# Optimization experiments

Hardware: AMD Instinct MI355X
Metric: run time of the kernel (lower is better)

The kernel has to match this reference:

```python
import jax, jax.numpy as jnp
import numpy as np

N_NODES = 100_000
E_OFF = 1_500_000
LATENT = 64
MP_STEPS = 3


def setup_inputs() -> dict:
    key = jax.random.key(0)
    ks = jax.random.split(key, 12)
    # lower-triangular graph: all self-loops + random off-diagonal edges with row >= col
    r = jax.random.randint(ks[0], (E_OFF,), 0, N_NODES)
    c = jax.random.randint(ks[1], (E_OFF,), 0, N_NODES)
    diag = jnp.arange(N_NODES)
    edge_row = jnp.concatenate([jnp.maximum(r, c), diag]).astype(jnp.int64)
    edge_col = jnp.concatenate([jnp.minimum(r, c), diag]).astype(jnp.int64)
    E = E_OFF + N_NODES
    # positive weights (gcn_norm takes deg^{-1/2} of weighted degree)
    edge_attr = jax.random.uniform(ks[2], (E,), jnp.float32) + 0.05
    x = jax.random.normal(ks[3], (N_NODES, 1), jnp.float32)
    L = LATENT
    def lin(k, fi, fo):
        return jax.random.normal(k, (fi, fo), jnp.float32) / np.sqrt(fi)
    return {
        "x": x,
        "edge_attr": edge_attr,
        "w_enc": lin(ks[4], 1, L), "b_enc": jnp.zeros((L,), jnp.float32),
        "conv1_w": jax.random.normal(ks[5], (MP_STEPS, L, L), jnp.float32) / np.sqrt(L),
        "conv1_b": jnp.zeros((MP_STEPS, L), jnp.float32),
        "conv2_w": jax.random.normal(ks[6], (MP_STEPS, L, L), jnp.float32) / np.sqrt(L),
        "conv2_b": jnp.zeros((MP_STEPS, L), jnp.float32),
        "dec_w1": lin(ks[7], 2 * L, L), "dec_b1": jnp.zeros((L,), jnp.float32),
        "dec_w2": lin(ks[8], L, 1), "dec_b2": jnp.zeros((1,), jnp.float32),
        "edge_row": edge_row,
        "edge_col": edge_col,
    }


def reference(x, edge_attr, w_enc, b_enc, conv1_w, conv1_b, conv2_w, conv2_b,
              dec_w1, dec_b1, dec_w2, dec_b2, edge_row, edge_col):
    N = x.shape[0]
    # GCN normalization (graph already contains all self-loops, so PyG's
    # add_remaining_self_loops is a no-op and keeps existing loop weights)
    deg = jax.ops.segment_sum(edge_attr, edge_col, num_segments=N)
    dinv = jnp.where(deg > 0, jax.lax.rsqrt(jnp.maximum(deg, 1e-30)), 0.0)
    norm = dinv[edge_row] * edge_attr * dinv[edge_col]  # [E]
    cnt = jnp.maximum(
        jax.ops.segment_sum(jnp.ones_like(edge_attr), edge_col, num_segments=N), 1.0
    )[:, None]  # mean aggregation denominator

    def gcn(h, W, b):
        m = (h @ W)[edge_row] * norm[:, None]           # [E, F] messages
        agg = jax.ops.segment_sum(m, edge_col, num_segments=N) / cnt
        return agg + b

    # node encoder: single Linear (no activation)
    h = x @ w_enc + b_enc
    for i in range(MP_STEPS):
        h = jax.nn.relu(gcn(h, conv1_w[i], conv1_b[i]))
        h = jax.nn.relu(gcn(h, conv2_w[i], conv2_b[i]))

    # edge decoder: gather endpoints, MLP [2L -> L -> 1]
    e = jnp.concatenate([h[edge_row], h[edge_col]], axis=1)
    e = jax.nn.relu(e @ dec_w1 + dec_b1)
    e = (e @ dec_w2 + dec_b2)[:, 0]                      # [E]
    vals = jnp.where(edge_row == edge_col, jax.nn.softplus(e), e)
    return vals
```

## Files before the change

### kernel.cpp

```cpp
#include <hip/hip_runtime.h>
#include <hip/hip_fp16.h>
#include <math.h>

#define L 64
#define FIXS 65536.0f
#define WAITCNT_LGKM0 0xC07F

#define FMAMIX_LO(acc, pkh, ws) \
    asm("v_fma_mix_f32 %0, %1, %2, %0 op_sel:[0,0,0] op_sel_hi:[1,0,0]" \
        : "+v"(acc) : "v"(pkh), "v"(ws))
#define FMAMIX_HI(acc, pkh, ws) \
    asm("v_fma_mix_f32 %0, %1, %2, %0 op_sel:[1,0,0] op_sel_hi:[1,0,0]" \
        : "+v"(acc) : "v"(pkh), "v"(ws))
#define PKADDRELU(d, a, b) \
    asm("v_pk_add_f16 %0, %1, %2\n\tv_pk_max_f16 %0, %0, 0" \
        : "=v"(d) : "v"(a), "v"(b))

#define GLOAD(xw_, qv_, J) \
    xw_ = (unsigned)__shfl((int)mwv, (J) * 8 + grp); \
    qv_ = h4[(size_t)(xw_ & 0x1FFFFu) * 8 + sub];
#define FMA8(A, qv_, xw_) { \
    float wv_ = __half2float(__ushort_as_half((unsigned short)((xw_) >> 17))); \
    FMAMIX_LO(A[0], (qv_).x, wv_); FMAMIX_HI(A[1], (qv_).x, wv_); \
    FMAMIX_LO(A[2], (qv_).y, wv_); FMAMIX_HI(A[3], (qv_).y, wv_); \
    FMAMIX_LO(A[4], (qv_).z, wv_); FMAMIX_HI(A[5], (qv_).z, wv_); \
    FMAMIX_LO(A[6], (qv_).w, wv_); FMAMIX_HI(A[7], (qv_).w, wv_); }


__global__ void k_hist(const int* __restrict__ col, const float* __restrict__ attr,
                       unsigned* __restrict__ degcnt,
                       int* __restrict__ rank, int E) {
    int e = blockIdx.x * blockDim.x + threadIdx.x;
    if (e < E) {
        int c = col[e];
        unsigned fx = (unsigned)(int)rintf(attr[e] * FIXS);
        unsigned old = atomicAdd(&degcnt[c], (1u << 24) | fx);
        rank[e] = (int)(old >> 24);
    }
}

__global__ void k_dinv(const unsigned* __restrict__ degcnt,
                       float* __restrict__ dinv, int* __restrict__ cntI,
                       float* __restrict__ rcnt, int N) {
    int n = blockIdx.x * blockDim.x + threadIdx.x;
    if (n < N) {
        unsigned p = degcnt[n];
        unsigned cnt = p >> 24;
        float d = (float)(p & 0xFFFFFFu) * (1.0f / FIXS);
        dinv[n] = (d > 0.f) ? (1.0f / sqrtf(fmaxf(d, 1e-30f))) : 0.f;
        cntI[n] = (int)cnt;
        unsigned c = cnt ? cnt : 1u;
        rcnt[n] = 1.0f / (float)c;
    }
}


__global__ __launch_bounds__(256) void k_scan_a(const int* __restrict__ cntI,
                                                int* __restrict__ blockSums, int N) {
    __shared__ int red[4];
    int b = blockIdx.x, t = threadIdx.x;
    int base = b * 1024 + t * 4;
    int s = 0;
    #pragma unroll
    for (int i = 0; i < 4; ++i) { int idx = base + i; if (idx < N) s += cntI[idx]; }
    #pragma unroll
    for (int off = 32; off > 0; off >>= 1) s += __shfl_down(s, off);
    if ((t & 63) == 0) red[t >> 6] = s;
    __syncthreads();
    if (t == 0) blockSums[b] = red[0] + red[1] + red[2] + red[3];
}

__global__ __launch_bounds__(1024) void k_scan_b(int* __restrict__ blockSums, int B,
                                                 int* __restrict__ ptr, int N) {
    __shared__ int sh[1024];
    int t = threadIdx.x;
    sh[t] = (t < B) ? blockSums[t] : 0;
    __syncthreads();
    for (int off = 1; off < 1024; off <<= 1) {
        int v = (t >= off) ? sh[t - off] : 0;
        __syncthreads();
        sh[t] += v;
        __syncthreads();
    }
    if (t < B) blockSums[t] = (t == 0) ? 0 : sh[t - 1];
    if (t == B - 1) ptr[N] = sh[t];
}

__global__ __launch_bounds__(256) void k_scan_c(const int* __restrict__ cntI,
                                                const int* __restrict__ blockSums,
                                                int* __restrict__ ptr, int N) {
    __shared__ int th[256];
    int b = blockIdx.x, t = threadIdx.x;
    int base = b * 1024 + t * 4;
    int v[4]; int s = 0;
    #pragma unroll
    for (int i = 0; i < 4; ++i) {
        int idx = base + i;
        v[i] = (idx < N) ? cntI[idx] : 0;
        s += v[i];
    }
    th[t] = s;
    __syncthreads();
    for (int off = 1; off < 256; off <<= 1) {
        int xv = (t >= off) ? th[t - off] : 0;
        __syncthreads();
        th[t] += xv;
        __syncthreads();
    }
    int pre = ((t == 0) ? 0 : th[t - 1]) + blockSums[b];
    #pragma unroll
    for (int i = 0; i < 4; ++i) {
        int idx = base + i;
        if (idx < N) ptr[idx] = pre;
        pre += v[i];
    }
}

__global__ void k_scatter(const int* __restrict__ row, const int* __restrict__ col,
                          const float* __restrict__ attr, const float* __restrict__ dinv,
                          const int* __restrict__ colptr,
                          int* __restrict__ rank,
                          unsigned* __restrict__ csrX, int E) {
    int e = blockIdx.x * blockDim.x + threadIdx.x;
    if (e < E) {
        int r = row[e], c = col[e];
        int pos = colptr[c] + rank[e];
        float nrm = dinv[r] * attr[e] * dinv[c];
        unsigned short nb = __half_as_ushort(__float2half(nrm));
        csrX[pos] = (unsigned)r | ((unsigned)nb << 17);
        rank[e] = pos;
    }
}


__global__ __launch_bounds__(256) void k_fill(const int* __restrict__ colptr,
                                              int* __restrict__ colof, int N) {
    int lane = threadIdx.x & 63;
    int wid  = (blockIdx.x * blockDim.x + threadIdx.x) >> 6;
    int nw   = (gridDim.x * blockDim.x) >> 6;
    for (int n = wid; n < N; n += nw) {
        int beg = colptr[n], end = colptr[n + 1];
        for (int p = beg + lane; p < end; p += 64) colof[p] = n;
    }
}


__global__ void k_encode(const float* __restrict__ x, const float* __restrict__ w_enc,
                         const float* __restrict__ b_enc, __half* __restrict__ h, int N) {
    int idx = blockIdx.x * blockDim.x + threadIdx.x;
    if (idx < N * L) {
        int n = idx >> 6, f = idx & 63;
        h[idx] = __float2half(x[n] * w_enc[f] + b_enc[f]);
    }
}


__global__ __launch_bounds__(256, 2) void k_gcn(const uint4* __restrict__ h4,
        __half* __restrict__ h_out,
        const float* __restrict__ W, const float* __restrict__ bias,
        const int* __restrict__ colptr, const unsigned* __restrict__ csrX,
        const float* __restrict__ rcnt, int N) {
    __shared__ float sm[4][72];
    int lane = threadIdx.x & 63;
    int warp = threadIdx.x >> 6;
    int grp  = lane >> 3;
    int sub  = lane & 7;
    int wid  = (blockIdx.x * blockDim.x + threadIdx.x) >> 6;
    int nw   = (gridDim.x * blockDim.x) >> 6;
    float* smw = &sm[warp][0];

    float Wc[L];
    #pragma unroll
    for (int f = 0; f < L; ++f) Wc[f] = W[f * L + lane];
    #pragma unroll
    for (int f = 0; f < L; ++f) asm volatile("" : "+v"(Wc[f]));
    float bl = bias[lane];

    int beg = 0, end = 0; unsigned mw = 0;
    if (wid < N) {
        beg = colptr[wid];
        end = colptr[wid + 1];
        if (beg + lane < end) mw = csrX[beg + lane];
    }

    for (int n = wid; n < N; n += nw) {
        int n2 = n + nw;
        int beg2 = 0, end2 = 0;
        if (n2 < N) { beg2 = colptr[n2]; end2 = colptr[n2 + 1]; }
        float rcv = rcnt[n];

        float va[8];
        #pragma unroll
        for (int i = 0; i < 8; ++i) va[i] = 0.f;

        auto PROC = [&](unsigned mwv, int mm) {
            int kmax = (mm + 7) >> 3;
            int k = 0;
            while (k < kmax) {
                int rem = kmax - k;
                if (rem >= 4) {
                    unsigned x0, x1, x2, x3; uint4 q0, q1, q2, q3;
                    GLOAD(x0, q0, k) GLOAD(x1, q1, k + 1)
                    GLOAD(x2, q2, k + 2) GLOAD(x3, q3, k + 3)
                    FMA8(va, q0, x0) FMA8(va, q1, x1)
                    FMA8(va, q2, x2) FMA8(va, q3, x3)
                    k += 4;
                } else if (rem == 3) {
                    unsigned x0, x1, x2; uint4 q0, q1, q2;
                    GLOAD(x0, q0, k) GLOAD(x1, q1, k + 1) GLOAD(x2, q2, k + 2)
                    FMA8(va, q0, x0) FMA8(va, q1, x1) FMA8(va, q2, x2)
                    k += 3;
                } else if (rem == 2) {
                    unsigned x0, x1; uint4 q0, q1;
                    GLOAD(x0, q0, k) GLOAD(x1, q1, k + 1)
                    FMA8(va, q0, x0) FMA8(va, q1, x1)
                    k += 2;
                } else {
                    unsigned x0; uint4 q0;
                    GLOAD(x0, q0, k)
                    FMA8(va, q0, x0)
                    k += 1;
                }
            }
        };

        int m = end - beg; if (m > 64) m = 64;
        PROC(mw, m);
        for (int base = beg + 64; base < end; base += 64) {
            int mm = end - base; if (mm > 64) mm = 64;
            unsigned mwc = 0;
            if (lane < mm) mwc = csrX[base + lane];
            PROC(mwc, mm);
        }

        unsigned mw2 = 0;
        if (n2 < N && beg2 + lane < end2) mw2 = csrX[beg2 + lane];

        float s[8];
        #pragma unroll
        for (int i = 0; i < 8; ++i) {
            float v = va[i];
            v += __shfl_xor(v, 8);
            v += __shfl_xor(v, 16);
            v += __shfl_xor(v, 32);
            s[i] = v;
        }
        if (lane < 8) {
            #pragma unroll
            for (int i = 0; i < 8; ++i) smw[8 * lane + i] = s[i];
        }
        __builtin_amdgcn_s_waitcnt(WAITCNT_LGKM0);
        float a0 = 0.f, a1 = 0.f, a2 = 0.f, a3 = 0.f;
        const float4* smv = (const float4*)smw;
        #pragma unroll
        for (int q = 0; q < 16; ++q) {
            float4 sv = smv[q];
            a0 += sv.x * Wc[4 * q + 0];
            a1 += sv.y * Wc[4 * q + 1];
            a2 += sv.z * Wc[4 * q + 2];
            a3 += sv.w * Wc[4 * q + 3];
        }
        float o = ((a0 + a1) + (a2 + a3)) * rcv + bl;
        h_out[(size_t)n * L + lane] = __float2half(fmaxf(o, 0.f));

        beg = beg2; end = end2; mw = mw2;
    }
}


__global__ __launch_bounds__(256, 2) void k_mv2(const __half* __restrict__ h,
        const float* __restrict__ W1, const float* __restrict__ b1,
        __half* __restrict__ U, __half* __restrict__ V, int N) {
    __shared__ float sm[4][72];
    int lane = threadIdx.x & 63;
    int warp = threadIdx.x >> 6;
    int wid  = (blockIdx.x * blockDim.x + threadIdx.x) >> 6;
    int nw   = (gridDim.x * blockDim.x) >> 6;
    float* smw = &sm[warp][0];
    float Wu[L], Wv[L];
    #pragma unroll
    for (int f = 0; f < L; ++f) Wu[f] = W1[f * L + lane];
    #pragma unroll
    for (int f = 0; f < L; ++f) Wv[f] = W1[(L + f) * L + lane];
    float bl = b1[lane];
    for (int n = wid; n < N; n += nw) {
        float hl = __half2float(h[(size_t)n * L + lane]);
        smw[lane] = hl;
        __builtin_amdgcn_s_waitcnt(WAITCNT_LGKM0);
        float a0 = 0.f, a1 = 0.f, c0 = 0.f, c1 = 0.f;
        const float4* smv = (const float4*)smw;
        #pragma unroll
        for (int q = 0; q < 16; ++q) {
            float4 sv = smv[q];
            a0 += sv.x * Wu[4 * q + 0] ; a1 += sv.y * Wu[4 * q + 1];
            a0 += sv.z * Wu[4 * q + 2] ; a1 += sv.w * Wu[4 * q + 3];
            c0 += sv.x * Wv[4 * q + 0] ; c1 += sv.y * Wv[4 * q + 1];
            c0 += sv.z * Wv[4 * q + 2] ; c1 += sv.w * Wv[4 * q + 3];
        }
        U[(size_t)n * L + lane] = __float2half((a0 + a1) + bl);
        V[(size_t)n * L + lane] = __float2half(c0 + c1);
        __builtin_amdgcn_s_waitcnt(WAITCNT_LGKM0);
    }
}


__global__ __launch_bounds__(256, 8) void k_edge(const __half* __restrict__ U,
        const __half* __restrict__ V, const float* __restrict__ w2,
        const float* __restrict__ b2, const unsigned* __restrict__ csrX,
        const int* __restrict__ colof, float* __restrict__ tmp, int E) {
    int sub = threadIdx.x & 7;
    float w2f[8];
    #pragma unroll
    for (int i = 0; i < 8; ++i) w2f[i] = w2[8 * sub + i];
    float b2v = b2[0];
    int tid = blockIdx.x * blockDim.x + threadIdx.x;
    int np  = (gridDim.x * blockDim.x) >> 3;
    for (int p = tid >> 3; p < E; p += np) {
        unsigned md = csrX[p];
        int r = (int)(md & 0x1FFFFu);
        int n = colof[p];
        uint4 uq = ((const uint4*)(U + (size_t)r * L))[sub];
        uint4 vq = ((const uint4*)(V + (size_t)n * L))[sub];
        float p0 = 0.f, p1 = 0.f;
        #define DOT2X(uw_, vw_, B) { unsigned t_; \
            PKADDRELU(t_, (uw_), (vw_)); \
            FMAMIX_LO(p0, t_, w2f[B]); FMAMIX_HI(p1, t_, w2f[(B) + 1]); }
        DOT2X(uq.x, vq.x, 0) DOT2X(uq.y, vq.y, 2)
        DOT2X(uq.z, vq.z, 4) DOT2X(uq.w, vq.w, 6)
        #undef DOT2X
        float pd = p0 + p1;
        pd += __shfl_xor(pd, 1);
        pd += __shfl_xor(pd, 2);
        pd += __shfl_xor(pd, 4);
        if (sub == 0) tmp[p] = pd + b2v;
    }
}


__global__ void k_perm(const int* __restrict__ epos, const float* __restrict__ tmp,
                       const int* __restrict__ erow, const int* __restrict__ ecol,
                       float* __restrict__ out, int E) {
    int e = blockIdx.x * blockDim.x + threadIdx.x;
    if (e < E) {
        float val = tmp[epos[e]];
        if (erow[e] == ecol[e])
            val = fmaxf(val, 0.f) + log1pf(expf(-fabsf(val)));
        out[e] = val;
    }
}


extern "C" void kernel_launch(void* const* d_in, const int* in_sizes, int n_in,
                              void* d_out, int out_size, void* d_ws, size_t ws_size,
                              hipStream_t stream) {
    const float* x     = (const float*)d_in[0];
    const float* attr  = (const float*)d_in[1];
    const float* w_enc = (const float*)d_in[2];
    const float* b_enc = (const float*)d_in[3];
    const float* c1w   = (const float*)d_in[4];
    const float* c1b   = (const float*)d_in[5];
    const float* c2w   = (const float*)d_in[6];
    const float* c2b   = (const float*)d_in[7];
    const float* dw1   = (const float*)d_in[8];
    const float* db1   = (const float*)d_in[9];
    const float* dw2   = (const float*)d_in[10];
    const float* db2   = (const float*)d_in[11];
    const int*   erow  = (const int*)d_in[12];
    const int*   ecol  = (const int*)d_in[13];
    int N = in_sizes[0];
    int E = in_sizes[1];
    float* out = (float*)d_out;

    char* w = (char*)d_ws;
    auto alloc = [&](size_t bytes) {
        char* p = w; w += (bytes + 255) & ~(size_t)255; return p;
    };
    unsigned* degcnt = (unsigned*)alloc((size_t)N * 4);
    size_t zbytes = (size_t)(w - (char*)d_ws);
    float* dinv   = (float*)alloc((size_t)N * 4);
    int*   cntI   = (int*)  alloc((size_t)N * 4);
    float* rcnt   = (float*)alloc((size_t)N * 4);
    int*   colptr = (int*)  alloc((size_t)(N + 1) * 4);
    int*   bsums  = (int*)  alloc(((size_t)(N + 1023) / 1024 + 1) * 4);
    int*   rank   = (int*)  alloc((size_t)E * 4);
    unsigned* csrX = (unsigned*)alloc((size_t)E * 4);
    int*   colof  = (int*)  alloc((size_t)E * 4);
    float* tmp    = (float*)alloc((size_t)E * 4);
    __half* hA    = (__half*)alloc((size_t)N * L * 2);
    __half* hB    = (__half*)alloc((size_t)N * L * 2);
    __half* hU    = (__half*)alloc((size_t)N * L * 2);
    __half* hV    = (__half*)alloc((size_t)N * L * 2);
    (void)ws_size; (void)n_in; (void)out_size;

    (void)hipMemsetAsync(d_ws, 0, zbytes, stream);

    int eb = (E + 255) / 256;
    int nb = (N + 255) / 256;
    int B  = (N + 1023) / 1024;
    k_hist<<<eb, 256, 0, stream>>>(ecol, attr, degcnt, rank, E);
    k_dinv<<<nb, 256, 0, stream>>>(degcnt, dinv, cntI, rcnt, N);
    k_scan_a<<<B, 256, 0, stream>>>(cntI, bsums, N);
    k_scan_b<<<1, 1024, 0, stream>>>(bsums, B, colptr, N);
    k_scan_c<<<B, 256, 0, stream>>>(cntI, bsums, colptr, N);
    k_scatter<<<eb, 256, 0, stream>>>(erow, ecol, attr, dinv, colptr, rank, csrX, E);
    k_fill<<<1024, 256, 0, stream>>>(colptr, colof, N);
    k_encode<<<(N * L + 255) / 256, 256, 0, stream>>>(x, w_enc, b_enc, hA, N);

    __half* hin = hA; __half* hout = hB;
    for (int i = 0; i < 3; ++i) {
        k_gcn<<<2048, 256, 0, stream>>>((const uint4*)hin, hout, c1w + i * L * L,
                                        c1b + i * L, colptr, csrX, rcnt, N);
        __half* t = hin; hin = hout; hout = t;
        k_gcn<<<2048, 256, 0, stream>>>((const uint4*)hin, hout, c2w + i * L * L,
                                        c2b + i * L, colptr, csrX, rcnt, N);
        t = hin; hin = hout; hout = t;
    }
    k_mv2<<<2048, 256, 0, stream>>>(hin, dw1, db1, hU, hV, N);
    k_edge<<<2048, 256, 0, stream>>>(hU, hV, dw2, db2, csrX, colof, tmp, E);
    k_perm<<<eb, 256, 0, stream>>>(rank, tmp, erow, ecol, out, E);
}
```

Baseline: 632.1 us.

## Reorder GCN to transform-then-aggregate with MFMA node matmul kernel

Each GCN layer is restructured from aggregate-then-multiply into a per-node dense transform (h@W) followed by a pure sparse aggregation, using the linearity of the weighted sum. The dense transform runs in a new MFMA kernel that splits W into hi/lo fp16 parts to keep accuracy, and the encoder is folded into the first layer's weights. The aggregation kernel drops its 64-float register weight cache and the shared-memory reduction, so it can run at higher occupancy. The cost is five extra kernel launches and an extra N×64 fp16 round trip through memory per layer, plus one more fp16 rounding of the transformed features before the gather.

```diff
diff --git a/kernel.cpp b/kernel.cpp
--- a/kernel.cpp
+++ b/kernel.cpp
@@ -5,6 +5,9 @@
 #define L 64
 #define FIXS 65536.0f
 #define WAITCNT_LGKM0 0xC07F
+
+typedef _Float16 f16x8 __attribute__((ext_vector_type(8)));
+typedef float f32x4 __attribute__((ext_vector_type(4)));
 
 #define FMAMIX_LO(acc, pkh, ws) \
     asm("v_fma_mix_f32 %0, %1, %2, %0 op_sel:[0,0,0] op_sel_hi:[1,0,0]" \
@@ -115,6 +118,7 @@
         pre += v[i];
     }
 }
+
 
 __global__ void k_scatter(const int* __restrict__ row, const int* __restrict__ col,
                           const float* __restrict__ attr, const float* __restrict__ dinv,
@@ -145,36 +149,44 @@
 }
 
 
-__global__ void k_encode(const float* __restrict__ x, const float* __restrict__ w_enc,
-                         const float* __restrict__ b_enc, __half* __restrict__ h, int N) {
+__global__ void k_fold(const float* __restrict__ w_enc, const float* __restrict__ b_enc,
+                       const float* __restrict__ W1,
+                       float* __restrict__ we1, float* __restrict__ be1) {
+    int j = threadIdx.x;
+    if (j < L) {
+        float a = 0.f, b = 0.f;
+        for (int f = 0; f < L; ++f) {
+            float wv = W1[f * L + j];
+            a += w_enc[f] * wv;
+            b += b_enc[f] * wv;
+        }
+        we1[j] = a; be1[j] = b;
+    }
+}
+
+__global__ void k_encode(const float* __restrict__ x, const float* __restrict__ we1,
+                         const float* __restrict__ be1, __half* __restrict__ g, int N) {
     int idx = blockIdx.x * blockDim.x + threadIdx.x;
     if (idx < N * L) {
         int n = idx >> 6, f = idx & 63;
-        h[idx] = __float2half(x[n] * w_enc[f] + b_enc[f]);
-    }
-}
-
-
-__global__ __launch_bounds__(256, 2) void k_gcn(const uint4* __restrict__ h4,
-        __half* __restrict__ h_out,
-        const float* __restrict__ W, const float* __restrict__ bias,
+        g[idx] = __float2half(x[n] * we1[f] + be1[f]);
+    }
+}
+
+
+__global__ __launch_bounds__(256, 6) void k_agg(const uint4* __restrict__ h4,
+        __half* __restrict__ h_out, const float* __restrict__ bias,
         const int* __restrict__ colptr, const unsigned* __restrict__ csrX,
         const float* __restrict__ rcnt, int N) {
-    __shared__ float sm[4][72];
     int lane = threadIdx.x & 63;
-    int warp = threadIdx.x >> 6;
     int grp  = lane >> 3;
     int sub  = lane & 7;
     int wid  = (blockIdx.x * blockDim.x + threadIdx.x) >> 6;
     int nw   = (gridDim.x * blockDim.x) >> 6;
-    float* smw = &sm[warp][0];
-
-    float Wc[L];
-    #pragma unroll
-    for (int f = 0; f < L; ++f) Wc[f] = W[f * L + lane];
-    #pragma unroll
-    for (int f = 0; f < L; ++f) asm volatile("" : "+v"(Wc[f]));
-    float bl = bias[lane];
+
+    float bl8[8];
+    #pragma unroll
+    for (int i = 0; i < 8; ++i) bl8[i] = bias[8 * sub + i];
 
     int beg = 0, end = 0; unsigned mw = 0;
     if (wid < N) {
@@ -246,24 +258,65 @@
             s[i] = v;
         }
         if (lane < 8) {
+            unsigned u[4];
             #pragma unroll
-            for (int i = 0; i < 8; ++i) smw[8 * lane + i] = s[i];
-        }
-        __builtin_amdgcn_s_waitcnt(WAITCNT_LGKM0);
-        float a0 = 0.f, a1 = 0.f, a2 = 0.f, a3 = 0.f;
-        const float4* smv = (const float4*)smw;
+            for (int i = 0; i < 4; ++i) {
+                float oa = fmaxf(s[2 * i]     * rcv + bl8[2 * i],     0.f);
+                float ob = fmaxf(s[2 * i + 1] * rcv + bl8[2 * i + 1], 0.f);
+                u[i] = (unsigned)__half_as_ushort(__float2half(oa))
+                     | ((unsigned)__half_as_ushort(__float2half(ob)) << 16);
+            }
+            uint4 st; st.x = u[0]; st.y = u[1]; st.z = u[2]; st.w = u[3];
+            ((uint4*)h_out)[(size_t)n * 8 + lane] = st;
+        }
+
+        beg = beg2; end = end2; mw = mw2;
+    }
+}
+
+
+__global__ __launch_bounds__(256) void k_gx(const __half* __restrict__ h,
+        const float* __restrict__ W, __half* __restrict__ g, int N) {
+    int lane = threadIdx.x & 63;
+    int wid  = (blockIdx.x * blockDim.x + threadIdx.x) >> 6;
+    int nw   = (gridDim.x * blockDim.x) >> 6;
+    int r16  = lane & 15;
+    int q4   = lane >> 4;
+
+    f16x8 bh[4][2], bl[4][2];
+    #pragma unroll
+    for (int t = 0; t < 4; ++t)
         #pragma unroll
-        for (int q = 0; q < 16; ++q) {
-            float4 sv = smv[q];
-            a0 += sv.x * Wc[4 * q + 0];
-            a1 += sv.y * Wc[4 * q + 1];
-            a2 += sv.z * Wc[4 * q + 2];
-            a3 += sv.w * Wc[4 * q + 3];
-        }
-        float o = ((a0 + a1) + (a2 + a3)) * rcv + bl;
-        h_out[(size_t)n * L + lane] = __float2half(fmaxf(o, 0.f));
-
-        beg = beg2; end = end2; mw = mw2;
+        for (int ks = 0; ks < 2; ++ks)
+            #pragma unroll
+            for (int i = 0; i < 8; ++i) {
+                int k = ks * 32 + q4 * 8 + i;
+                float wv = W[k * L + t * 16 + r16];
+                _Float16 hi = (_Float16)wv;
+                bh[t][ks][i] = hi;
+                bl[t][ks][i] = (_Float16)(wv - (float)hi);
+            }
+
+    int tiles = (N + 15) >> 4;
+    for (int tt = wid; tt < tiles; tt += nw) {
+        int n0 = tt << 4;
+        int row = n0 + r16; if (row >= N) row = N - 1;
+        f16x8 a0 = *(const f16x8*)(h + (size_t)row * L + q4 * 8);
+        f16x8 a1 = *(const f16x8*)(h + (size_t)row * L + 32 + q4 * 8);
+        #pragma unroll
+        for (int t = 0; t < 4; ++t) {
+            f32x4 acc = {0.f, 0.f, 0.f, 0.f};
+            acc = __builtin_amdgcn_mfma_f32_16x16x32_f16(a0, bl[t][0], acc, 0, 0, 0);
+            acc = __builtin_amdgcn_mfma_f32_16x16x32_f16(a1, bl[t][1], acc, 0, 0, 0);
+            acc = __builtin_amdgcn_mfma_f32_16x16x32_f16(a0, bh[t][0], acc, 0, 0, 0);
+            acc = __builtin_amdgcn_mfma_f32_16x16x32_f16(a1, bh[t][1], acc, 0, 0, 0);
+            #pragma unroll
+            for (int r = 0; r < 4; ++r) {
+                int node = n0 + q4 * 4 + r;
+                if (node < N)
+                    g[(size_t)node * L + t * 16 + r16] = __float2half(acc[r]);
+            }
+        }
     }
 }
 
@@ -382,6 +435,8 @@
     float* rcnt   = (float*)alloc((size_t)N * 4);
     int*   colptr = (int*)  alloc((size_t)(N + 1) * 4);
     int*   bsums  = (int*)  alloc(((size_t)(N + 1023) / 1024 + 1) * 4);
+    float* we1    = (float*)alloc(L * 4);
+    float* be1    = (float*)alloc(L * 4);
     int*   rank   = (int*)  alloc((size_t)E * 4);
     unsigned* csrX = (unsigned*)alloc((size_t)E * 4);
     int*   colof  = (int*)  alloc((size_t)E * 4);
@@ -390,6 +445,7 @@
     __half* hB    = (__half*)alloc((size_t)N * L * 2);
     __half* hU    = (__half*)alloc((size_t)N * L * 2);
     __half* hV    = (__half*)alloc((size_t)N * L * 2);
+    __half* gbuf  = hU;
     (void)ws_size; (void)n_in; (void)out_size;
 
     (void)hipMemsetAsync(d_ws, 0, zbytes, stream);
@@ -404,18 +460,27 @@
     k_scan_c<<<B, 256, 0, stream>>>(cntI, bsums, colptr, N);
     k_scatter<<<eb, 256, 0, stream>>>(erow, ecol, attr, dinv, colptr, rank, csrX, E);
     k_fill<<<1024, 256, 0, stream>>>(colptr, colof, N);
-    k_encode<<<(N * L + 255) / 256, 256, 0, stream>>>(x, w_enc, b_enc, hA, N);
-
-    __half* hin = hA; __half* hout = hB;
-    for (int i = 0; i < 3; ++i) {
-        k_gcn<<<2048, 256, 0, stream>>>((const uint4*)hin, hout, c1w + i * L * L,
-                                        c1b + i * L, colptr, csrX, rcnt, N);
-        __half* t = hin; hin = hout; hout = t;
-        k_gcn<<<2048, 256, 0, stream>>>((const uint4*)hin, hout, c2w + i * L * L,
-                                        c2b + i * L, colptr, csrX, rcnt, N);
-        t = hin; hin = hout; hout = t;
-    }
-    k_mv2<<<2048, 256, 0, stream>>>(hin, dw1, db1, hU, hV, N);
+
+    k_fold<<<1, 64, 0, stream>>>(w_enc, b_enc, c1w, we1, be1);
+    k_encode<<<(N * L + 255) / 256, 256, 0, stream>>>(x, we1, be1, gbuf, N);
+
+    const float* Ws[6] = {c1w,             c2w,
+                          c1w + L * L,     c2w + L * L,
+                          c1w + 2 * L * L, c2w + 2 * L * L};
+    const float* Bs[6] = {c1b,         c2b,
+                          c1b + L,     c2b + L,
+                          c1b + 2 * L, c2b + 2 * L};
+    (void)Ws[0];
+    __half* outs[2] = {hA, hB};
+    __half* hcur = nullptr;
+    for (int j = 0; j < 6; ++j) {
+        hcur = outs[j & 1];
+        k_agg<<<2048, 256, 0, stream>>>((const uint4*)gbuf, hcur, Bs[j],
+                                        colptr, csrX, rcnt, N);
+        if (j < 5)
+            k_gx<<<512, 256, 0, stream>>>(hcur, Ws[j + 1], gbuf, N);
+    }
+    k_mv2<<<2048, 256, 0, stream>>>(hcur, dw1, db1, hU, hV, N);
     k_edge<<<2048, 256, 0, stream>>>(hU, hV, dw2, db2, csrX, colof, tmp, E);
     k_perm<<<eb, 256, 0, stream>>>(rank, tmp, erow, ecol, out, E);
 }
```

Result: faster. 583.2 us (-7.7%).
